# Optimization experiments

Hardware: AMD Instinct MI355X
Metric: run time of the kernel (lower is better)

Reference implementation:

```python
import jax, jax.numpy as jnp
import numpy as np

N = 100000
E = 1600000
D_IN = 128
D_H = 128


def setup_inputs() -> dict:
    key = jax.random.key(0)
    ks = jax.random.split(key, 10)
    x = jax.random.normal(ks[0], (N, D_IN), dtype=jnp.float32)
    src = jax.random.randint(ks[1], (E,), 0, N)
    dst = jax.random.randint(ks[2], (E,), 0, N)
    s1 = 1.0 / np.sqrt(D_IN)
    s2 = 1.0 / np.sqrt(D_H)
    W_self1 = jax.random.uniform(ks[3], (D_H, D_IN), jnp.float32, -s1, s1)
    W_neigh1 = jax.random.uniform(ks[4], (D_H, D_IN), jnp.float32, -s1, s1)
    b1 = jnp.zeros((D_H,), jnp.float32)
    W_self2 = jax.random.uniform(ks[5], (D_H, D_H), jnp.float32, -s2, s2)
    W_neigh2 = jax.random.uniform(ks[6], (D_H, D_H), jnp.float32, -s2, s2)
    b2 = jnp.zeros((D_H,), jnp.float32)
    return {"x": x, "src": src, "dst": dst,
            "W_self1": W_self1, "W_neigh1": W_neigh1, "b1": b1,
            "W_self2": W_self2, "W_neigh2": W_neigh2, "b2": b2}


def _sage_conv(h, src, dst, W_self, W_neigh, b):
    n = h.shape[0]
    msg = h[src]  # [E, d] gather of source node features
    agg = jax.ops.segment_sum(msg, dst, num_segments=n)  # [N, d]
    deg = jax.ops.segment_sum(jnp.ones((src.shape[0],), h.dtype), dst, num_segments=n)
    h_neigh = agg / jnp.maximum(deg, 1.0)[:, None]  # mean; isolated nodes -> 0
    return h @ W_self.T + h_neigh @ W_neigh.T + b


def reference(x, src, dst, W_self1, W_neigh1, b1, W_self2, W_neigh2, b2):
    h = _sage_conv(x, src, dst, W_self1, W_neigh1, b1)
    h = jax.nn.relu(h)
    h = _sage_conv(h, src, dst, W_self2, W_neigh2, b2)
    return h
```

## Files before the change

### kernel.cpp

```cpp
#include <hip/hip_runtime.h>


typedef unsigned int uint;
typedef unsigned short ushort;
typedef unsigned char uchar;
using short8 = __attribute__((ext_vector_type(8))) short;
using f32x4  = __attribute__((ext_vector_type(4))) float;

__device__ __forceinline__ float bflo(uint u) { return __uint_as_float(u << 16); }
__device__ __forceinline__ float bfhi(uint u) { return __uint_as_float(u & 0xffff0000u); }
__device__ __forceinline__ ushort f2bf(float f) {
  uint u = __float_as_uint(f);
  return (ushort)((u + 0x7fffu + ((u >> 16) & 1u)) >> 16);
}

#define EPB 4096
#define NBKT_MAX 512
#define SLAB_CAP 5120

__global__ __launch_bounds__(256) void f32_to_bf16_kernel(
    const float* __restrict__ in, ushort* __restrict__ out, int n4) {
  int i = blockIdx.x * 256 + threadIdx.x;
  if (i >= n4) return;
  float4 v = ((const float4*)in)[i];
  ushort4 r;
  r.x = f2bf(v.x); r.y = f2bf(v.y); r.z = f2bf(v.z); r.w = f2bf(v.w);
  ((ushort4*)out)[i] = r;
}

__global__ __launch_bounds__(256) void w_to_bf16_kernel(
    const float* __restrict__ w0, const float* __restrict__ w1,
    const float* __restrict__ w2, const float* __restrict__ w3,
    ushort* __restrict__ o0, ushort* __restrict__ o1,
    ushort* __restrict__ o2, ushort* __restrict__ o3, int n4) {
  int i = blockIdx.x * 256 + threadIdx.x;
  if (i >= n4) return;
  const float* in = (blockIdx.y == 0) ? w0 : (blockIdx.y == 1) ? w1
                    : (blockIdx.y == 2) ? w2 : w3;
  ushort* out = (blockIdx.y == 0) ? o0 : (blockIdx.y == 1) ? o1
                : (blockIdx.y == 2) ? o2 : o3;
  float4 v = ((const float4*)in)[i];
  ushort4 r;
  r.x = f2bf(v.x); r.y = f2bf(v.y); r.z = f2bf(v.z); r.w = f2bf(v.w);
  ((ushort4*)out)[i] = r;
}

template <int IN_F32>
__global__ __launch_bounds__(256) void quant_rows_kernel(
    const void* __restrict__ in_, uchar* __restrict__ outq,
    float* __restrict__ scales, int n) {
  int node = (blockIdx.x * 256 + threadIdx.x) >> 5;
  int lane = threadIdx.x & 31;
  if (node >= n) return;
  float f[4];
  if (IN_F32) {
    float4 v = *(const float4*)((const float*)in_ + (size_t)node * 128 + lane * 4);
    f[0] = v.x; f[1] = v.y; f[2] = v.z; f[3] = v.w;
  } else {
    uint2 v = *(const uint2*)((const ushort*)in_ + (size_t)node * 128 + lane * 4);
    f[0] = bflo(v.x); f[1] = bfhi(v.x); f[2] = bflo(v.y); f[3] = bfhi(v.y);
  }
  float mx = fmaxf(fmaxf(fabsf(f[0]), fabsf(f[1])),
                   fmaxf(fabsf(f[2]), fabsf(f[3])));
#pragma unroll
  for (int off = 1; off < 32; off <<= 1) mx = fmaxf(mx, __shfl_xor(mx, off, 64));
  float inv = (mx > 0.f) ? 127.0f / mx : 0.f;
  uint q0 = (uint)(__float2int_rn(f[0] * inv) + 128);
  uint q1 = (uint)(__float2int_rn(f[1] * inv) + 128);
  uint q2 = (uint)(__float2int_rn(f[2] * inv) + 128);
  uint q3 = (uint)(__float2int_rn(f[3] * inv) + 128);
  uint packed = q0 | (q1 << 8) | (q2 << 16) | (q3 << 24);
  *(uint*)(outq + (size_t)node * 128 + lane * 4) = packed;
  if (lane == 0) scales[node] = (mx > 0.f) ? mx / 127.0f : 0.f;
}

__global__ __launch_bounds__(256) void partition_kernel(
    const int* __restrict__ src, const int* __restrict__ dst,
    int* __restrict__ bktcnt, uint* __restrict__ gpart, int E, int nbkt) {
  __shared__ uint staged[EPB];
  __shared__ ushort stagedb[EPB];
  __shared__ int hist[NBKT_MAX];
  __shared__ int scanex[NBKT_MAX];
  __shared__ int lcur[NBKT_MAX];
  __shared__ int gbase[NBKT_MAX];
  __shared__ int s2[256];
  const int t = threadIdx.x;
  const int e0 = blockIdx.x * EPB;
  const int total = min(EPB, E - e0);

  hist[t] = 0; hist[t + 256] = 0;
  __syncthreads();

  int myb[16];
  uint myu[16];
#pragma unroll
  for (int q = 0; q < 16; ++q) {
    int e = e0 + q * 256 + t;
    if (e < E) {
      int s = src[e], d = dst[e];
      myb[q] = d >> 8;
      myu[q] = (uint)s | ((uint)(d & 255) << 24);
      atomicAdd(&hist[myb[q]], 1);
    } else {
      myb[q] = -1;
      myu[q] = 0;
    }
  }
  __syncthreads();

  int h0 = hist[2 * t], h1 = hist[2 * t + 1];
  s2[t] = h0 + h1;
  __syncthreads();
  for (int off = 1; off < 256; off <<= 1) {
    int v = (t >= off) ? s2[t - off] : 0;
    __syncthreads();
    s2[t] += v;
    __syncthreads();
  }
  int ex2 = s2[t] - (h0 + h1);
  scanex[2 * t] = ex2;
  scanex[2 * t + 1] = ex2 + h0;
  lcur[2 * t] = ex2;
  lcur[2 * t + 1] = ex2 + h0;
  __syncthreads();

#pragma unroll
  for (int q = 0; q < 2; ++q) {
    int b = t + q * 256;
    int c = hist[b];
    gbase[b] = (b < nbkt && c > 0)
                   ? (b * SLAB_CAP + atomicAdd(&bktcnt[b], c))
                   : 0;
  }

#pragma unroll
  for (int q = 0; q < 16; ++q) {
    if (myb[q] >= 0) {
      int p = atomicAdd(&lcur[myb[q]], 1);
      staged[p] = myu[q];
      stagedb[p] = (ushort)myb[q];
    }
  }
  __syncthreads();

  for (int i = t; i < total; i += 256) {
    int b = stagedb[i];
    gpart[gbase[b] + (i - scanex[b])] = staged[i];
  }
}

__global__ __launch_bounds__(512) void bucket_scan_kernel(
    const int* __restrict__ bktcnt, int* __restrict__ bucket_base,
    int* __restrict__ row_start, int nbkt, int n, int E) {
  __shared__ int sh[512];
  int t = threadIdx.x;
  int v = (t < nbkt) ? bktcnt[t] : 0;
  sh[t] = v;
  __syncthreads();
  for (int off = 1; off < 512; off <<= 1) {
    int u = (t >= off) ? sh[t - off] : 0;
    __syncthreads();
    sh[t] += u;
    __syncthreads();
  }
  if (t < nbkt) bucket_base[t] = sh[t] - v;
  if (t == 0) row_start[n] = E;
}

__global__ __launch_bounds__(256) void fine_fill_kernel(
    const uint* __restrict__ gpart, const int* __restrict__ bktcnt,
    const int* __restrict__ bucket_base, int* __restrict__ row_start,
    int* __restrict__ csr, int n) {
  __shared__ int hist[256];
  __shared__ int pfx[256];
  __shared__ int lcur[256];
  const int b = blockIdx.x;
  const int t = threadIdx.x;
  const int cnt = bktcnt[b];
  const uint* sl = gpart + (size_t)b * SLAB_CAP;
  hist[t] = 0;
  __syncthreads();
  for (int i = t; i < cnt; i += 256) atomicAdd(&hist[sl[i] >> 24], 1);
  __syncthreads();
  int h = hist[t];
  pfx[t] = h;
  __syncthreads();
  for (int off = 1; off < 256; off <<= 1) {
    int u = (t >= off) ? pfx[t - off] : 0;
    __syncthreads();
    pfx[t] += u;
    __syncthreads();
  }
  const int base = bucket_base[b] + pfx[t] - h;
  const int n0 = b << 8;
  if (n0 + t < n) row_start[n0 + t] = base;
  lcur[t] = base;
  __syncthreads();
  for (int i = t; i < cnt; i += 256) {
    uint u = sl[i];
    int p = atomicAdd(&lcur[u >> 24], 1);
    csr[p] = (int)(u & 0xFFFFFFu);
  }
}

__global__ __launch_bounds__(256) void aggregate_mean_i8_kernel(
    const uchar* __restrict__ hq, const float* __restrict__ scales,
    const int* __restrict__ csr, const int* __restrict__ row_start,
    ushort* __restrict__ outb, int n) {
  int node = (blockIdx.x * 256 + threadIdx.x) >> 5;
  int lane = threadIdx.x & 31;
  if (node >= n) return;
  const int sub = lane >> 4;
  const int dlo = (lane & 15) * 8;
  int e0 = row_start[node], e1 = row_start[node + 1];
  float a0 = 0.f, a1 = 0.f, a2 = 0.f, a3 = 0.f;
  float a4 = 0.f, a5 = 0.f, a6 = 0.f, a7 = 0.f;
  if (e1 > e0) {
    const int elast = e1 - 1;
    float csum = 0.f;
    for (int j0 = e0; j0 < e1; j0 += 8) {
      uint2 v[4];
      float sm[4];
#pragma unroll
      for (int q = 0; q < 4; ++q) {
        int j = j0 + 2 * q + sub;
        int jc = (j <= elast) ? j : elast;
        int s = csr[jc];
        v[q] = *(const uint2*)(hq + (size_t)s * 128 + dlo);
        float m = (j <= elast) ? 1.0f : 0.0f;
        sm[q] = m * scales[s];
      }
#pragma unroll
      for (int q = 0; q < 4; ++q) {
        const uint lo = v[q].x, hi = v[q].y;
        const float s_ = sm[q];
        a0 = fmaf((float)(lo & 255), s_, a0);
        a1 = fmaf((float)((lo >> 8) & 255), s_, a1);
        a2 = fmaf((float)((lo >> 16) & 255), s_, a2);
        a3 = fmaf((float)(lo >> 24), s_, a3);
        a4 = fmaf((float)(hi & 255), s_, a4);
        a5 = fmaf((float)((hi >> 8) & 255), s_, a5);
        a6 = fmaf((float)((hi >> 16) & 255), s_, a6);
        a7 = fmaf((float)(hi >> 24), s_, a7);
        csum += s_;
      }
    }
    const float c128 = 128.0f * csum;
    a0 -= c128; a1 -= c128; a2 -= c128; a3 -= c128;
    a4 -= c128; a5 -= c128; a6 -= c128; a7 -= c128;
    a0 += __shfl_xor(a0, 16, 64);
    a1 += __shfl_xor(a1, 16, 64);
    a2 += __shfl_xor(a2, 16, 64);
    a3 += __shfl_xor(a3, 16, 64);
    a4 += __shfl_xor(a4, 16, 64);
    a5 += __shfl_xor(a5, 16, 64);
    a6 += __shfl_xor(a6, 16, 64);
    a7 += __shfl_xor(a7, 16, 64);
    float inv = 1.0f / (float)(e1 - e0);
    a0 *= inv; a1 *= inv; a2 *= inv; a3 *= inv;
    a4 *= inv; a5 *= inv; a6 *= inv; a7 *= inv;
  }
  if (lane < 16) {
    uint4 r;
    r.x = (uint)f2bf(a0) | ((uint)f2bf(a1) << 16);
    r.y = (uint)f2bf(a2) | ((uint)f2bf(a3) << 16);
    r.z = (uint)f2bf(a4) | ((uint)f2bf(a5) << 16);
    r.w = (uint)f2bf(a6) | ((uint)f2bf(a7) << 16);
    *(uint4*)(outb + (size_t)node * 128 + dlo) = r;
  }
}

template <int RELU, int OUT_BF16>
__global__ __launch_bounds__(256, 4) void sage_gemm_mfma_kernel(
    const ushort* __restrict__ hs, const ushort* __restrict__ hn,
    const ushort* __restrict__ Wsb, const ushort* __restrict__ Wnb,
    const float* __restrict__ bias, void* __restrict__ out_, int n) {
  const int w = threadIdx.x >> 6;
  const int lane = threadIdx.x & 63;
  const int lr = lane & 15;
  const int lk = (lane >> 4) * 8;
  const int m0 = blockIdx.x * 64;
  if (m0 >= n) return;

  short8 bs[2][4], bn[2][4];
  float bv[2];
  int oc[2];
#pragma unroll
  for (int u = 0; u < 2; ++u) {
    oc[u] = (w + u * 4) * 16 + lr;
    const ushort* qs = Wsb + (size_t)oc[u] * 128 + lk;
    const ushort* qn = Wnb + (size_t)oc[u] * 128 + lk;
#pragma unroll
    for (int s = 0; s < 4; ++s) {
      bs[u][s] = *(const short8*)(qs + s * 32);
      bn[u][s] = *(const short8*)(qn + s * 32);
    }
    bv[u] = bias[oc[u]];
  }

  const int nmt = min(4, (n - m0 + 15) >> 4);
  for (int mt = 0; mt < nmt; ++mt) {
    short8 as[4], an[4];
    {
      int arow = m0 + mt * 16 + lr;
      if (arow >= n) arow = n - 1;
      const ushort* ps = hs + (size_t)arow * 128 + lk;
      const ushort* pq = hn + (size_t)arow * 128 + lk;
#pragma unroll
      for (int s = 0; s < 4; ++s) {
        as[s] = *(const short8*)(ps + s * 32);
        an[s] = *(const short8*)(pq + s * 32);
      }
    }
    const int mbase = m0 + mt * 16 + (lane >> 4) * 4;
#pragma unroll
    for (int u = 0; u < 2; ++u) {
      f32x4 acc = {0.f, 0.f, 0.f, 0.f};
#pragma unroll
      for (int s = 0; s < 4; ++s)
        acc = __builtin_amdgcn_mfma_f32_16x16x32_bf16(as[s], bs[u][s], acc, 0, 0, 0);
#pragma unroll
      for (int s = 0; s < 4; ++s)
        acc = __builtin_amdgcn_mfma_f32_16x16x32_bf16(an[s], bn[u][s], acc, 0, 0, 0);
#pragma unroll
      for (int r = 0; r < 4; ++r) {
        int node = mbase + r;
        if (node < n) {
          float v = acc[r] + bv[u];
          if (RELU) v = fmaxf(v, 0.f);
          if (OUT_BF16)
            ((ushort*)out_)[(size_t)node * 128 + oc[u]] = f2bf(v);
          else
            ((float*)out_)[(size_t)node * 128 + oc[u]] = v;
        }
      }
    }
  }
}

extern "C" void kernel_launch(void* const* d_in, const int* in_sizes, int n_in,
                              void* d_out, int out_size, void* d_ws, size_t ws_size,
                              hipStream_t stream) {
  const float* x   = (const float*)d_in[0];
  const int*   src = (const int*)d_in[1];
  const int*   dst = (const int*)d_in[2];
  const float* Ws1 = (const float*)d_in[3];
  const float* Wn1 = (const float*)d_in[4];
  const float* b1  = (const float*)d_in[5];
  const float* Ws2 = (const float*)d_in[6];
  const float* Wn2 = (const float*)d_in[7];
  const float* b2  = (const float*)d_in[8];
  float* out = (float*)d_out;
  const int D = 128;
  const int N = in_sizes[0] / D;
  const int E = in_sizes[1];
  (void)n_in; (void)out_size; (void)ws_size;

  char* p = (char*)d_ws;
  auto carve = [&](size_t bytes) {
    char* r = p;
    p += (bytes + 255) & ~(size_t)255;
    return r;
  };
  int*    bktcnt      = (int*)carve(NBKT_MAX * 4);
  int*    bucket_base = (int*)carve(NBKT_MAX * 4);
  int*    row_start   = (int*)carve((size_t)(N + 1) * 4);
  uint*   gpart       = (uint*)carve((size_t)NBKT_MAX * SLAB_CAP * 4);
  int*    csr         = (int*)carve((size_t)E * 4);
  ushort* xb          = (ushort*)carve((size_t)N * D * 2);
  ushort* h1b         = (ushort*)carve((size_t)N * D * 2);
  ushort* hnb         = (ushort*)carve((size_t)N * D * 2);
  float*  xs          = (float*)carve((size_t)N * 4);
  float*  h1s         = (float*)carve((size_t)N * 4);
  ushort* Wsb1        = (ushort*)carve((size_t)D * D * 2);
  ushort* Wnb1        = (ushort*)carve((size_t)D * D * 2);
  ushort* Wsb2        = (ushort*)carve((size_t)D * D * 2);
  ushort* Wnb2        = (ushort*)carve((size_t)D * D * 2);
  uchar* xq  = (uchar*)h1b;
  uchar* h1q = (uchar*)xb;

  hipMemsetAsync(bktcnt, 0, NBKT_MAX * 4, stream);

  const int nbkt = (N + 255) >> 8;
  const int wq = D * D / 4;

  f32_to_bf16_kernel<<<(N * D / 4 + 255) / 256, 256, 0, stream>>>(x, xb, N * D / 4);
  {
    dim3 g((wq + 255) / 256, 4);
    w_to_bf16_kernel<<<g, 256, 0, stream>>>(Ws1, Wn1, Ws2, Wn2,
                                            Wsb1, Wnb1, Wsb2, Wnb2, wq);
  }
  quant_rows_kernel<1><<<(N + 7) / 8, 256, 0, stream>>>(x, xq, xs, N);

  partition_kernel<<<(E + EPB - 1) / EPB, 256, 0, stream>>>(src, dst, bktcnt, gpart, E, nbkt);
  bucket_scan_kernel<<<1, 512, 0, stream>>>(bktcnt, bucket_base, row_start, nbkt, N, E);
  fine_fill_kernel<<<nbkt, 256, 0, stream>>>(gpart, bktcnt, bucket_base, row_start, csr, N);

  const int gblocks = (N + 63) / 64;

  aggregate_mean_i8_kernel<<<(N + 7) / 8, 256, 0, stream>>>(xq, xs, csr, row_start, hnb, N);
  sage_gemm_mfma_kernel<1, 1><<<gblocks, 256, 0, stream>>>(
      xb, hnb, Wsb1, Wnb1, b1, h1b, N);

  quant_rows_kernel<0><<<(N + 7) / 8, 256, 0, stream>>>(h1b, h1q, h1s, N);

  aggregate_mean_i8_kernel<<<(N + 7) / 8, 256, 0, stream>>>(h1q, h1s, csr, row_start, hnb, N);
  sage_gemm_mfma_kernel<0, 0><<<gblocks, 256, 0, stream>>>(
      h1b, hnb, Wsb2, Wnb2, b2, out, N);
}
```

Before: 235.8 us.

## Store bf16 activations and weights in MFMA fragment-tiled layout

Converts x, weights, aggregated neighbours and the hidden layer into a 16-row tile layout that matches the MFMA operand fragments. The GEMM can then load each operand as contiguous 16-byte per-lane reads instead of strided row reads. Producers (conversion, aggregation, layer-1 GEMM output) and the quantizer are rewritten to read and write the new layout. The layer-1 GEMM's bf16 output now lands as scattered 2-byte stores into the tiled layout, and every consumer has to compute more complex addresses.

```diff
diff --git a/kernel.cpp b/kernel.cpp
--- a/kernel.cpp
+++ b/kernel.cpp
@@ -18,31 +18,50 @@
 #define NBKT_MAX 512
 #define SLAB_CAP 5120
 
-__global__ __launch_bounds__(256) void f32_to_bf16_kernel(
-    const float* __restrict__ in, ushort* __restrict__ out, int n4) {
-  int i = blockIdx.x * 256 + threadIdx.x;
-  if (i >= n4) return;
-  float4 v = ((const float4*)in)[i];
-  ushort4 r;
-  r.x = f2bf(v.x); r.y = f2bf(v.y); r.z = f2bf(v.z); r.w = f2bf(v.w);
-  ((ushort4*)out)[i] = r;
-}
-
-__global__ __launch_bounds__(256) void w_to_bf16_kernel(
+
+__global__ __launch_bounds__(256) void x_to_frag_kernel(
+    const float* __restrict__ x, ushort* __restrict__ xf, int n) {
+  const int tile = blockIdx.x;
+  const int s = threadIdx.x >> 6;
+  const int l = threadIdx.x & 63;
+  const int row = tile * 16 + (l & 15);
+  const int k = s * 32 + (l >> 4) * 8;
+  ushort4 r0 = {0, 0, 0, 0}, r1 = {0, 0, 0, 0};
+  if (row < n) {
+    const float* p = x + (size_t)row * 128 + k;
+    float4 a = ((const float4*)p)[0];
+    float4 b = ((const float4*)p)[1];
+    r0.x = f2bf(a.x); r0.y = f2bf(a.y); r0.z = f2bf(a.z); r0.w = f2bf(a.w);
+    r1.x = f2bf(b.x); r1.y = f2bf(b.y); r1.z = f2bf(b.z); r1.w = f2bf(b.w);
+  }
+  ushort* dp = xf + (size_t)tile * 2048 + s * 512 + l * 8;
+  *(ushort4*)dp = r0;
+  *(ushort4*)(dp + 4) = r1;
+}
+
+__global__ __launch_bounds__(256) void w_to_frag_kernel(
     const float* __restrict__ w0, const float* __restrict__ w1,
     const float* __restrict__ w2, const float* __restrict__ w3,
     ushort* __restrict__ o0, ushort* __restrict__ o1,
-    ushort* __restrict__ o2, ushort* __restrict__ o3, int n4) {
-  int i = blockIdx.x * 256 + threadIdx.x;
-  if (i >= n4) return;
+    ushort* __restrict__ o2, ushort* __restrict__ o3) {
   const float* in = (blockIdx.y == 0) ? w0 : (blockIdx.y == 1) ? w1
                     : (blockIdx.y == 2) ? w2 : w3;
   ushort* out = (blockIdx.y == 0) ? o0 : (blockIdx.y == 1) ? o1
                 : (blockIdx.y == 2) ? o2 : o3;
-  float4 v = ((const float4*)in)[i];
-  ushort4 r;
-  r.x = f2bf(v.x); r.y = f2bf(v.y); r.z = f2bf(v.z); r.w = f2bf(v.w);
-  ((ushort4*)out)[i] = r;
+  const int tile = blockIdx.x;
+  const int s = threadIdx.x >> 6;
+  const int l = threadIdx.x & 63;
+  const int row = tile * 16 + (l & 15);
+  const int k = s * 32 + (l >> 4) * 8;
+  const float* p = in + (size_t)row * 128 + k;
+  float4 a = ((const float4*)p)[0];
+  float4 b = ((const float4*)p)[1];
+  ushort4 r0, r1;
+  r0.x = f2bf(a.x); r0.y = f2bf(a.y); r0.z = f2bf(a.z); r0.w = f2bf(a.w);
+  r1.x = f2bf(b.x); r1.y = f2bf(b.y); r1.z = f2bf(b.z); r1.w = f2bf(b.w);
+  ushort* dp = out + (size_t)tile * 2048 + s * 512 + l * 8;
+  *(ushort4*)dp = r0;
+  *(ushort4*)(dp + 4) = r1;
 }
 
 template <int IN_F32>
@@ -57,7 +76,11 @@
     float4 v = *(const float4*)((const float*)in_ + (size_t)node * 128 + lane * 4);
     f[0] = v.x; f[1] = v.y; f[2] = v.z; f[3] = v.w;
   } else {
-    uint2 v = *(const uint2*)((const ushort*)in_ + (size_t)node * 128 + lane * 4);
+    const ushort* hp = (const ushort*)in_ + (size_t)(node >> 4) * 2048 +
+                       (lane >> 3) * 512 +
+                       (((lane >> 1) & 3) * 16 + (node & 15)) * 8 +
+                       (lane & 1) * 4;
+    uint2 v = *(const uint2*)hp;
     f[0] = bflo(v.x); f[1] = bfhi(v.x); f[2] = bflo(v.y); f[3] = bfhi(v.y);
   }
   float mx = fmaxf(fmaxf(fabsf(f[0]), fabsf(f[1])),
@@ -206,7 +229,7 @@
 __global__ __launch_bounds__(256) void aggregate_mean_i8_kernel(
     const uchar* __restrict__ hq, const float* __restrict__ scales,
     const int* __restrict__ csr, const int* __restrict__ row_start,
-    ushort* __restrict__ outb, int n) {
+    ushort* __restrict__ outf, int n) {
   int node = (blockIdx.x * 256 + threadIdx.x) >> 5;
   int lane = threadIdx.x & 31;
   if (node >= n) return;
@@ -266,53 +289,53 @@
     r.y = (uint)f2bf(a2) | ((uint)f2bf(a3) << 16);
     r.z = (uint)f2bf(a4) | ((uint)f2bf(a5) << 16);
     r.w = (uint)f2bf(a6) | ((uint)f2bf(a7) << 16);
-    *(uint4*)(outb + (size_t)node * 128 + dlo) = r;
-  }
-}
-
-template <int RELU, int OUT_BF16>
+    ushort* dp = outf + (size_t)(node >> 4) * 2048 + (lane >> 2) * 512 +
+                 ((lane & 3) * 16 + (node & 15)) * 8;
+    *(uint4*)dp = r;
+  }
+}
+
+template <int RELU, int OUT_FRAG>
 __global__ __launch_bounds__(256, 4) void sage_gemm_mfma_kernel(
     const ushort* __restrict__ hs, const ushort* __restrict__ hn,
-    const ushort* __restrict__ Wsb, const ushort* __restrict__ Wnb,
+    const ushort* __restrict__ Wsf, const ushort* __restrict__ Wnf,
     const float* __restrict__ bias, void* __restrict__ out_, int n) {
   const int w = threadIdx.x >> 6;
   const int lane = threadIdx.x & 63;
   const int lr = lane & 15;
-  const int lk = (lane >> 4) * 8;
   const int m0 = blockIdx.x * 64;
   if (m0 >= n) return;
 
   short8 bs[2][4], bn[2][4];
   float bv[2];
-  int oc[2];
 #pragma unroll
   for (int u = 0; u < 2; ++u) {
-    oc[u] = (w + u * 4) * 16 + lr;
-    const ushort* qs = Wsb + (size_t)oc[u] * 128 + lk;
-    const ushort* qn = Wnb + (size_t)oc[u] * 128 + lk;
+    const int ot = w + u * 4;
+    const ushort* qs = Wsf + (size_t)ot * 2048 + lane * 8;
+    const ushort* qn = Wnf + (size_t)ot * 2048 + lane * 8;
 #pragma unroll
     for (int s = 0; s < 4; ++s) {
-      bs[u][s] = *(const short8*)(qs + s * 32);
-      bn[u][s] = *(const short8*)(qn + s * 32);
-    }
-    bv[u] = bias[oc[u]];
+      bs[u][s] = *(const short8*)(qs + s * 512);
+      bn[u][s] = *(const short8*)(qn + s * 512);
+    }
+    bv[u] = bias[ot * 16 + lr];
   }
 
   const int nmt = min(4, (n - m0 + 15) >> 4);
   for (int mt = 0; mt < nmt; ++mt) {
+    const int tile = (m0 >> 4) + mt;
     short8 as[4], an[4];
     {
-      int arow = m0 + mt * 16 + lr;
-      if (arow >= n) arow = n - 1;
-      const ushort* ps = hs + (size_t)arow * 128 + lk;
-      const ushort* pq = hn + (size_t)arow * 128 + lk;
+      const ushort* ps = hs + (size_t)tile * 2048 + lane * 8;
+      const ushort* pq = hn + (size_t)tile * 2048 + lane * 8;
 #pragma unroll
       for (int s = 0; s < 4; ++s) {
-        as[s] = *(const short8*)(ps + s * 32);
-        an[s] = *(const short8*)(pq + s * 32);
+        as[s] = *(const short8*)(ps + s * 512);
+        an[s] = *(const short8*)(pq + s * 512);
       }
     }
-    const int mbase = m0 + mt * 16 + (lane >> 4) * 4;
+    const int rbase = (lane >> 4) * 4;
+    const int mbase = m0 + mt * 16 + rbase;
 #pragma unroll
     for (int u = 0; u < 2; ++u) {
       f32x4 acc = {0.f, 0.f, 0.f, 0.f};
@@ -322,16 +345,20 @@
 #pragma unroll
       for (int s = 0; s < 4; ++s)
         acc = __builtin_amdgcn_mfma_f32_16x16x32_bf16(an[s], bn[u][s], acc, 0, 0, 0);
+      const int ot = w + u * 4;
+      const size_t cu = (size_t)(ot >> 1) * 512 +
+                        (((ot & 1) * 2 + (lr >> 3)) * 16) * 8 + (lr & 7);
 #pragma unroll
       for (int r = 0; r < 4; ++r) {
         int node = mbase + r;
         if (node < n) {
           float v = acc[r] + bv[u];
           if (RELU) v = fmaxf(v, 0.f);
-          if (OUT_BF16)
-            ((ushort*)out_)[(size_t)node * 128 + oc[u]] = f2bf(v);
-          else
-            ((float*)out_)[(size_t)node * 128 + oc[u]] = v;
+          if (OUT_FRAG) {
+            ((ushort*)out_)[(size_t)tile * 2048 + (rbase + r) * 8 + cu] = f2bf(v);
+          } else {
+            ((float*)out_)[(size_t)node * 128 + ot * 16 + lr] = v;
+          }
         }
       }
     }
@@ -356,6 +383,8 @@
   const int E = in_sizes[1];
   (void)n_in; (void)out_size; (void)ws_size;
 
+  const int tiles = (N + 15) >> 4;
+
   char* p = (char*)d_ws;
   auto carve = [&](size_t bytes) {
     char* r = p;
@@ -367,28 +396,27 @@
   int*    row_start   = (int*)carve((size_t)(N + 1) * 4);
   uint*   gpart       = (uint*)carve((size_t)NBKT_MAX * SLAB_CAP * 4);
   int*    csr         = (int*)carve((size_t)E * 4);
-  ushort* xb          = (ushort*)carve((size_t)N * D * 2);
-  ushort* h1b         = (ushort*)carve((size_t)N * D * 2);
-  ushort* hnb         = (ushort*)carve((size_t)N * D * 2);
+  ushort* xbf         = (ushort*)carve((size_t)tiles * 2048 * 2);
+  ushort* h1f         = (ushort*)carve((size_t)tiles * 2048 * 2);
+  ushort* hnf         = (ushort*)carve((size_t)tiles * 2048 * 2);
   float*  xs          = (float*)carve((size_t)N * 4);
   float*  h1s         = (float*)carve((size_t)N * 4);
-  ushort* Wsb1        = (ushort*)carve((size_t)D * D * 2);
-  ushort* Wnb1        = (ushort*)carve((size_t)D * D * 2);
-  ushort* Wsb2        = (ushort*)carve((size_t)D * D * 2);
-  ushort* Wnb2        = (ushort*)carve((size_t)D * D * 2);
-  uchar* xq  = (uchar*)h1b;
-  uchar* h1q = (uchar*)xb;
+  ushort* Wf1s        = (ushort*)carve((size_t)D * D * 2);
+  ushort* Wf1n        = (ushort*)carve((size_t)D * D * 2);
+  ushort* Wf2s        = (ushort*)carve((size_t)D * D * 2);
+  ushort* Wf2n        = (ushort*)carve((size_t)D * D * 2);
+  uchar* xq  = (uchar*)h1f;
+  uchar* h1q = (uchar*)xbf;
 
   hipMemsetAsync(bktcnt, 0, NBKT_MAX * 4, stream);
 
   const int nbkt = (N + 255) >> 8;
-  const int wq = D * D / 4;
-
-  f32_to_bf16_kernel<<<(N * D / 4 + 255) / 256, 256, 0, stream>>>(x, xb, N * D / 4);
+
+  x_to_frag_kernel<<<tiles, 256, 0, stream>>>(x, xbf, N);
   {
-    dim3 g((wq + 255) / 256, 4);
-    w_to_bf16_kernel<<<g, 256, 0, stream>>>(Ws1, Wn1, Ws2, Wn2,
-                                            Wsb1, Wnb1, Wsb2, Wnb2, wq);
+    dim3 g(8, 4);
+    w_to_frag_kernel<<<g, 256, 0, stream>>>(Ws1, Wn1, Ws2, Wn2,
+                                            Wf1s, Wf1n, Wf2s, Wf2n);
   }
   quant_rows_kernel<1><<<(N + 7) / 8, 256, 0, stream>>>(x, xq, xs, N);
 
@@ -398,13 +426,13 @@
 
   const int gblocks = (N + 63) / 64;
 
-  aggregate_mean_i8_kernel<<<(N + 7) / 8, 256, 0, stream>>>(xq, xs, csr, row_start, hnb, N);
+  aggregate_mean_i8_kernel<<<(N + 7) / 8, 256, 0, stream>>>(xq, xs, csr, row_start, hnf, N);
   sage_gemm_mfma_kernel<1, 1><<<gblocks, 256, 0, stream>>>(
-      xb, hnb, Wsb1, Wnb1, b1, h1b, N);
-
-  quant_rows_kernel<0><<<(N + 7) / 8, 256, 0, stream>>>(h1b, h1q, h1s, N);
-
-  aggregate_mean_i8_kernel<<<(N + 7) / 8, 256, 0, stream>>>(h1q, h1s, csr, row_start, hnb, N);
+      xbf, hnf, Wf1s, Wf1n, b1, h1f, N);
+
+  quant_rows_kernel<0><<<(N + 7) / 8, 256, 0, stream>>>(h1f, h1q, h1s, N);
+
+  aggregate_mean_i8_kernel<<<(N + 7) / 8, 256, 0, stream>>>(h1q, h1s, csr, row_start, hnf, N);
   sage_gemm_mfma_kernel<0, 0><<<gblocks, 256, 0, stream>>>(
-      h1b, hnb, Wsb2, Wnb2, b2, out, N);
-}
+      h1f, hnf, Wf2s, Wf2n, b2, out, N);
+}
```

Result: faster. 206.2 us (-12.5%).
